# Performance work log

Measured on AMD Instinct MI355X. Metric: run time of the kernel, lower is better.

Reference implementation:

```python
import jax, jax.numpy as jnp
import numpy as np

ENC_H = 512      # encoder_hidden_dim -> encoder_out feature = 2*ENC_H
DEC_H = 512      # decoder_hidden_dim
B, S = 32, 2048  # batch, max_seq_len


def setup_inputs() -> dict:
    key = jax.random.key(0)
    k1, k2, k3, k4, k5, k6, k7 = jax.random.split(key, 7)
    encoder_out = jax.random.normal(k1, (B, S, 2 * ENC_H), dtype=jnp.float32)
    hidden = jax.random.normal(k2, (B, DEC_H), dtype=jnp.float32)
    lengths = jax.random.randint(k3, (B,), 1, S + 1, dtype=jnp.int64)
    in_dim = 2 * ENC_H + DEC_H
    # torch nn.Linear default init scale
    attn_w = jax.random.uniform(k4, (DEC_H, in_dim), jnp.float32, -1.0, 1.0) / np.sqrt(in_dim)
    attn_b = jax.random.uniform(k5, (DEC_H,), jnp.float32, -1.0, 1.0) / np.sqrt(in_dim)
    v_w = jax.random.uniform(k6, (1, DEC_H), jnp.float32, -1.0, 1.0) / np.sqrt(DEC_H)
    v_b = jax.random.uniform(k7, (1,), jnp.float32, -1.0, 1.0) / np.sqrt(DEC_H)
    return {"encoder_out": encoder_out, "hidden": hidden, "lengths": lengths,
            "attn_w": attn_w, "attn_b": attn_b, "v_w": v_w, "v_b": v_b}


def reference(encoder_out, hidden, lengths, attn_w, attn_b, v_w, v_b):
    # encoder_out: [B,S,2E], hidden: [B,D], lengths: [B]
    Bc, Sc, _ = encoder_out.shape
    h = jnp.broadcast_to(hidden[:, None, :], (Bc, Sc, hidden.shape[-1]))
    temp = jnp.concatenate([h, encoder_out], axis=2)           # [B,S,D+2E]
    e = jnp.tanh(jnp.einsum('bsf,df->bsd', temp, attn_w) + attn_b)  # [B,S,D]
    scores = jnp.einsum('bsd,d->bs', e, v_w[0]) + v_b[0]       # [B,S]
    mask = jnp.arange(Sc)[None, :] < lengths[:, None]          # [B,S]
    scores = jnp.where(mask, scores, -jnp.inf)
    energy = jax.nn.softmax(scores, axis=1)                    # softmax over valid positions
    energy = jnp.where(mask, energy, 0.0)                      # padded positions stay exactly 0
    context = jnp.einsum('bs,bse->be', energy, encoder_out)    # [B,2E]
    return context
```

## Files before the change

### kernel.cpp

```cpp
#include <hip/hip_runtime.h>
#include <hip/hip_bf16.h>
#include <math.h>

typedef __attribute__((ext_vector_type(4))) short short4v;
typedef __attribute__((ext_vector_type(8))) short short8;
typedef __attribute__((ext_vector_type(16))) float f32x16;

static constexpr int B  = 32;
static constexpr int S  = 2048;
static constexpr int D  = 512;
static constexpr int KE = 1024;
static constexpr int IN = 1536;

__device__ __forceinline__ unsigned pk2(float lo, float hi) {
    __hip_bfloat162 t = __float22bfloat162_rn(make_float2(lo, hi));
    unsigned u;
    __builtin_memcpy(&u, &t, 4);
    return u;
}

__device__ __forceinline__ short4v pack4(float4 f) {
    unsigned u2[2] = { pk2(f.x, f.y), pk2(f.z, f.w) };
    short4v r;
    __builtin_memcpy(&r, u2, 8);
    return r;
}

__device__ __forceinline__ short8 pack8(float4 f0, float4 f1) {
    unsigned u[4] = { pk2(f0.x, f0.y), pk2(f0.z, f0.w), pk2(f1.x, f1.y), pk2(f1.z, f1.w) };
    short8 r;
    __builtin_memcpy(&r, u, 16);
    return r;
}

__device__ __forceinline__ short8 cat44(short4v lo, short4v hi) {
    short8 r;
    __builtin_memcpy(&r, &lo, 8);
    __builtin_memcpy(((char*)&r) + 8, &hi, 8);
    return r;
}

__device__ __forceinline__ float tanh_fast(float x) {
    float e = __expf(2.0f * x);
    return (e - 1.0f) * __builtin_amdgcn_rcpf(e + 1.0f);
}

__global__ void k_prep(const float* __restrict__ attn_w,
                       const float* __restrict__ hidden,
                       const float* __restrict__ attn_b,
                       unsigned short* __restrict__ Bf,
                       float* __restrict__ u) {
    if (blockIdx.x < 256) {
        int o = blockIdx.x * 256 + threadIdx.x;
        int l6  = o & 63;
        int grp = o >> 6;
        int d = (grp & 15) * 32 + (l6 & 31);
        int k = (grp >> 4) * 16 + (l6 >> 5) * 8;
        const float* src = attn_w + (size_t)d * IN + 512 + k;
        float4 f0 = *(const float4*)src;
        float4 f1 = *(const float4*)(src + 4);
        ((short8*)Bf)[o] = pack8(f0, f1);
    } else {
        int gid = (blockIdx.x - 256) * 256 + threadIdx.x;
        int b = gid >> 9;
        int d = gid & (D - 1);
        const float* h = hidden + b * D;
        const float* w = attn_w + (size_t)d * IN;
        float acc = attn_b[d];
        for (int k = 0; k < D; k += 4) {
            float4 hv = *(const float4*)(h + k);
            float4 wv = *(const float4*)(w + k);
            acc += hv.x * wv.x + hv.y * wv.y + hv.z * wv.z + hv.w * wv.w;
        }
        u[gid] = acc;
    }
}

#define LOADB(K, DST) do {                                     \
    _Pragma("unroll")                                          \
    for (int _jt = 0; _jt < 4; _jt++)                          \
        DST[_jt] = bb[(size_t)(K) * 1024 + _jt * 64];          \
} while (0)

__global__ __launch_bounds__(256, 2) void k_fused(
    const float* __restrict__ enc, const unsigned short* __restrict__ Bfrag,
    const float* __restrict__ u, const float* __restrict__ v_w,
    const float* __restrict__ v_b, const int* __restrict__ lengths,
    float* __restrict__ num, float* __restrict__ den)
{
    __shared__ short4v ldsA[2][64 * 19];
    __shared__ float sPart[4][64];
    __shared__ float sExp[64];

    const int b   = blockIdx.y;
    const int s0  = blockIdx.x * 64;
    const int len = lengths[b];
    if (s0 >= len) return;

    const int tid = threadIdx.x;
    const int w   = tid >> 6;
    const int l   = tid & 63;

    const float* encb = enc + ((size_t)b * S + s0) * KE;
    const int mr = tid >> 4;
    const int cw = tid & 15;
    const float* aG = encb + (size_t)mr * KE + cw * 4;
    const int wbase = mr * 19 + cw;

    const short8* bb = (const short8*)Bfrag + (w * 4) * 64 + l;

    f32x16 acc[2][4];
    #pragma unroll
    for (int mt = 0; mt < 2; mt++)
        #pragma unroll
        for (int jt = 0; jt < 4; jt++)
            #pragma unroll
            for (int e = 0; e < 16; e++) acc[mt][jt][e] = 0.f;

    short8 pb[2][4];
    LOADB(0, pb[0]);
    LOADB(1, pb[1]);

    float4 g[4];
    #pragma unroll
    for (int i = 0; i < 4; i++) g[i] = *(const float4*)(aG + (size_t)i * 16 * KE);

    const int rb0 = (l & 31) * 19 + (l >> 5) * 2;
    const int rb1 = rb0 + 32 * 19;

    #pragma unroll 1
    for (int c = 0; c <= 16; ++c) {
        __syncthreads();
        if (c < 16) {
            #pragma unroll
            for (int i = 0; i < 4; i++)
                ldsA[c & 1][wbase + i * 16 * 19] = pack4(g[i]);
            if (c < 15) {
                #pragma unroll
                for (int i = 0; i < 4; i++)
                    g[i] = *(const float4*)(aG + (size_t)i * 16 * KE + (c + 1) * 64);
            }
        }
        if (c > 0) {
            const int buf = (c - 1) & 1;
            #pragma unroll
            for (int t2 = 0; t2 < 4; ++t2) {
                const short4v* base = &ldsA[buf][t2 * 4];
                short8 a0 = cat44(base[rb0], base[rb0 + 1]);
                short8 a1 = cat44(base[rb1], base[rb1 + 1]);
                const int bp = t2 & 1;
                #pragma unroll
                for (int jt = 0; jt < 4; jt++) {
                    acc[0][jt] = __builtin_amdgcn_mfma_f32_32x32x16_bf16(a0, pb[bp][jt], acc[0][jt], 0, 0, 0);
                    acc[1][jt] = __builtin_amdgcn_mfma_f32_32x32x16_bf16(a1, pb[bp][jt], acc[1][jt], 0, 0, 0);
                }
                LOADB(((c - 1) * 4 + t2 + 2) & 63, pb[bp]);
            }
        }
    }

    float vv[4], uu[4];
    const float* ub = u + b * D;
    #pragma unroll
    for (int jt = 0; jt < 4; jt++) {
        int d = w * 128 + jt * 32 + (l & 31);
        vv[jt] = v_w[d];
        uu[jt] = ub[d];
    }
    float red[2][16];
    #pragma unroll
    for (int mt = 0; mt < 2; mt++)
        #pragma unroll
        for (int r = 0; r < 16; r++) {
            float s = 0.f;
            #pragma unroll
            for (int jt = 0; jt < 4; jt++)
                s += vv[jt] * tanh_fast(acc[mt][jt][r] + uu[jt]);
            red[mt][r] = s;
        }
    #pragma unroll
    for (int off = 16; off >= 1; off >>= 1)
        #pragma unroll
        for (int mt = 0; mt < 2; mt++)
            #pragma unroll
            for (int r = 0; r < 16; r++)
                red[mt][r] += __shfl_xor(red[mt][r], off);
    if ((l & 31) == 0) {
        int hb = (l >> 5) * 4;
        #pragma unroll
        for (int mt = 0; mt < 2; mt++)
            #pragma unroll
            for (int r = 0; r < 16; r++)
                sPart[w][mt * 32 + (r & 3) + 8 * (r >> 2) + hb] = red[mt][r];
    }
    __syncthreads();

    if (tid < 64) {
        float sc = sPart[0][tid] + sPart[1][tid] + sPart[2][tid] + sPart[3][tid] + v_b[0];
        float wexp = (s0 + tid < len) ? __expf(sc) : 0.f;
        sExp[tid] = wexp;
        #pragma unroll
        for (int off = 32; off >= 1; off >>= 1) wexp += __shfl_xor(wexp, off);
        if (tid == 0) atomicAdd(den + b, wexp);
    }
    __syncthreads();

    const float4* e4 = (const float4*)encb;
    float4 cacc[4];
    #pragma unroll
    for (int j = 0; j < 4; j++) cacc[j] = make_float4(0.f, 0.f, 0.f, 0.f);
    #pragma unroll
    for (int i = 0; i < 16; i++) {
        #pragma unroll
        for (int j = 0; j < 4; j++) {
            float wgt = sExp[i * 4 + j];
            float4 v = e4[(size_t)(i * 4 + j) * 256 + tid];
            cacc[j].x += wgt * v.x; cacc[j].y += wgt * v.y;
            cacc[j].z += wgt * v.z; cacc[j].w += wgt * v.w;
        }
    }
    #pragma unroll
    for (int j = 1; j < 4; j++) {
        cacc[0].x += cacc[j].x; cacc[0].y += cacc[j].y;
        cacc[0].z += cacc[j].z; cacc[0].w += cacc[j].w;
    }
    float* o = num + b * KE + tid * 4;
    atomicAdd(o + 0, cacc[0].x);
    atomicAdd(o + 1, cacc[0].y);
    atomicAdd(o + 2, cacc[0].z);
    atomicAdd(o + 3, cacc[0].w);
}

__global__ void k_norm(const float* __restrict__ num, const float* __restrict__ den,
                       float* __restrict__ out) {
    int b = blockIdx.x;
    int t = threadIdx.x;
    float inv = 1.f / den[b];
    float4 v = ((const float4*)(num + b * KE))[t];
    v.x *= inv; v.y *= inv; v.z *= inv; v.w *= inv;
    ((float4*)(out + b * KE))[t] = v;
}

extern "C" void kernel_launch(void* const* d_in, const int* in_sizes, int n_in,
                              void* d_out, int out_size, void* d_ws, size_t ws_size,
                              hipStream_t stream) {
    const float* enc    = (const float*)d_in[0];
    const float* hidden = (const float*)d_in[1];
    const int*   lengths= (const int*)d_in[2];
    const float* attn_w = (const float*)d_in[3];
    const float* attn_b = (const float*)d_in[4];
    const float* v_w    = (const float*)d_in[5];
    const float* v_b    = (const float*)d_in[6];
    float* out = (float*)d_out;

    float* ws  = (float*)d_ws;
    float* u   = ws;
    float* num = u + B * D;
    float* den = num + B * KE;
    unsigned short* Bf = (unsigned short*)(den + 32);

    (void)hipMemsetAsync(num, 0, (size_t)(B * KE + B) * sizeof(float), stream);
    k_prep <<<dim3(320), 256, 0, stream>>>(attn_w, hidden, attn_b, Bf, u);
    k_fused<<<dim3(S / 64, B), 256, 0, stream>>>(enc, Bf, u, v_w, v_b, lengths, num, den);
    k_norm <<<dim3(B), 256, 0, stream>>>(num, den, out);
}
```

Before: 438.8 us.

## Stream encoder tiles into LDS via global_load_lds and coalesce hidden projection

The fused kernel now copies fp32 encoder tiles straight from global memory into a double-buffered, XOR-swizzled LDS buffer using async global_load_lds. The bf16 conversion moves to after the LDS read, which removes the register staging and the pack-then-store step, and the loop prologue/epilogue is simplified. Separately, the hidden·W projection in k_prep is restructured so that 16 lanes cooperatively read contiguous weight rows and combine results with a shuffle reduction, replacing the per-thread strided row loop. The cost is twice the LDS footprint, since tiles are stored as fp32, which could affect occupancy. Correctness also relies on the barrier waiting for the async LDS writes to complete.

```diff
diff --git a/kernel.cpp b/kernel.cpp
--- a/kernel.cpp
+++ b/kernel.cpp
@@ -2,7 +2,6 @@
 #include <hip/hip_bf16.h>
 #include <math.h>
 
-typedef __attribute__((ext_vector_type(4))) short short4v;
 typedef __attribute__((ext_vector_type(8))) short short8;
 typedef __attribute__((ext_vector_type(16))) float f32x16;
 
@@ -19,13 +18,6 @@
     return u;
 }
 
-__device__ __forceinline__ short4v pack4(float4 f) {
-    unsigned u2[2] = { pk2(f.x, f.y), pk2(f.z, f.w) };
-    short4v r;
-    __builtin_memcpy(&r, u2, 8);
-    return r;
-}
-
 __device__ __forceinline__ short8 pack8(float4 f0, float4 f1) {
     unsigned u[4] = { pk2(f0.x, f0.y), pk2(f0.z, f0.w), pk2(f1.x, f1.y), pk2(f1.z, f1.w) };
     short8 r;
@@ -33,16 +25,15 @@
     return r;
 }
 
-__device__ __forceinline__ short8 cat44(short4v lo, short4v hi) {
-    short8 r;
-    __builtin_memcpy(&r, &lo, 8);
-    __builtin_memcpy(((char*)&r) + 8, &hi, 8);
-    return r;
-}
-
 __device__ __forceinline__ float tanh_fast(float x) {
     float e = __expf(2.0f * x);
     return (e - 1.0f) * __builtin_amdgcn_rcpf(e + 1.0f);
+}
+
+typedef const __attribute__((address_space(1))) unsigned int guint;
+typedef __attribute__((address_space(3))) unsigned int luint;
+__device__ __forceinline__ void gload_lds16(const void* g, void* l) {
+    __builtin_amdgcn_global_load_lds((guint*)g, (luint*)l, 16, 0, 0);
 }
 
 __global__ void k_prep(const float* __restrict__ attn_w,
@@ -61,18 +52,31 @@
         float4 f1 = *(const float4*)(src + 4);
         ((short8*)Bf)[o] = pack8(f0, f1);
     } else {
-        int gid = (blockIdx.x - 256) * 256 + threadIdx.x;
-        int b = gid >> 9;
-        int d = gid & (D - 1);
+        int bx = blockIdx.x - 256;
+        int b  = bx >> 1;
+        int dh = bx & 1;
+        int w  = threadIdx.x >> 6;
+        int l  = threadIdx.x & 63;
+        int j  = l & 15;
+        int dsub = l >> 4;
         const float* h = hidden + b * D;
-        const float* w = attn_w + (size_t)d * IN;
-        float acc = attn_b[d];
-        for (int k = 0; k < D; k += 4) {
-            float4 hv = *(const float4*)(h + k);
-            float4 wv = *(const float4*)(w + k);
-            acc += hv.x * wv.x + hv.y * wv.y + hv.z * wv.z + hv.w * wv.w;
-        }
-        u[gid] = acc;
+        float4 hv[8];
+        #pragma unroll
+        for (int i = 0; i < 8; i++) hv[i] = *(const float4*)(h + i * 64 + j * 4);
+        #pragma unroll
+        for (int p = 0; p < 16; p++) {
+            int d = dh * 256 + p * 16 + w * 4 + dsub;
+            const float* wr = attn_w + (size_t)d * IN + j * 4;
+            float a = 0.f;
+            #pragma unroll
+            for (int i = 0; i < 8; i++) {
+                float4 wv = *(const float4*)(wr + i * 64);
+                a += hv[i].x * wv.x + hv[i].y * wv.y + hv[i].z * wv.z + hv[i].w * wv.w;
+            }
+            #pragma unroll
+            for (int off = 8; off >= 1; off >>= 1) a += __shfl_xor(a, off);
+            if (j == 0) u[b * D + d] = a + attn_b[d];
+        }
     }
 }
 
@@ -88,7 +92,7 @@
     const float* __restrict__ v_b, const int* __restrict__ lengths,
     float* __restrict__ num, float* __restrict__ den)
 {
-    __shared__ short4v ldsA[2][64 * 19];
+    __shared__ float4 ldsA[2][1024];
     __shared__ float sPart[4][64];
     __shared__ float sExp[64];
 
@@ -102,10 +106,10 @@
     const int l   = tid & 63;
 
     const float* encb = enc + ((size_t)b * S + s0) * KE;
-    const int mr = tid >> 4;
-    const int cw = tid & 15;
-    const float* aG = encb + (size_t)mr * KE + cw * 4;
-    const int wbase = mr * 19 + cw;
+
+    const int rsub = l >> 4;
+    const int xorv = (l & 15) ^ (w * 4 + rsub);
+    const float* aSrc = encb + (size_t)(w * 4 + rsub) * KE + 4 * xorv;
 
     const short8* bb = (const short8*)Bfrag + (w * 4) * 64 + l;
 
@@ -121,41 +125,43 @@
     LOADB(0, pb[0]);
     LOADB(1, pb[1]);
 
-    float4 g[4];
-    #pragma unroll
-    for (int i = 0; i < 4; i++) g[i] = *(const float4*)(aG + (size_t)i * 16 * KE);
-
-    const int rb0 = (l & 31) * 19 + (l >> 5) * 2;
-    const int rb1 = rb0 + 32 * 19;
+    const int m0  = l & 31;
+    const int x15 = m0 & 15;
+    const int hi2 = (l >> 5) * 2;
+
+    #pragma unroll
+    for (int i = 0; i < 4; i++)
+        gload_lds16(aSrc + (size_t)i * 16 * KE, (void*)&ldsA[0][(i * 4 + w) * 64]);
 
     #pragma unroll 1
-    for (int c = 0; c <= 16; ++c) {
+    for (int c = 0; c < 16; ++c) {
         __syncthreads();
-        if (c < 16) {
+        if (c < 15) {
+            const float* src = aSrc + (c + 1) * 64;
+            float4* bufn = ldsA[(c + 1) & 1];
             #pragma unroll
             for (int i = 0; i < 4; i++)
-                ldsA[c & 1][wbase + i * 16 * 19] = pack4(g[i]);
-            if (c < 15) {
-                #pragma unroll
-                for (int i = 0; i < 4; i++)
-                    g[i] = *(const float4*)(aG + (size_t)i * 16 * KE + (c + 1) * 64);
+                gload_lds16(src + (size_t)i * 16 * KE, (void*)&bufn[(i * 4 + w) * 64]);
+        }
+        const float4* bf = (const float4*)ldsA[c & 1];
+        #pragma unroll
+        for (int t2 = 0; t2 < 4; ++t2) {
+            const int sq = t2 * 4 + hi2;
+            const int p0 = sq ^ x15;
+            const int p1 = (sq + 1) ^ x15;
+            float4 f00 = bf[m0 * 16 + p0];
+            float4 f01 = bf[m0 * 16 + p1];
+            float4 f10 = bf[(m0 + 32) * 16 + p0];
+            float4 f11 = bf[(m0 + 32) * 16 + p1];
+            short8 a0 = pack8(f00, f01);
+            short8 a1 = pack8(f10, f11);
+            const int bp = t2 & 1;
+            #pragma unroll
+            for (int jt = 0; jt < 4; jt++) {
+                acc[0][jt] = __builtin_amdgcn_mfma_f32_32x32x16_bf16(a0, pb[bp][jt], acc[0][jt], 0, 0, 0);
+                acc[1][jt] = __builtin_amdgcn_mfma_f32_32x32x16_bf16(a1, pb[bp][jt], acc[1][jt], 0, 0, 0);
             }
-        }
-        if (c > 0) {
-            const int buf = (c - 1) & 1;
-            #pragma unroll
-            for (int t2 = 0; t2 < 4; ++t2) {
-                const short4v* base = &ldsA[buf][t2 * 4];
-                short8 a0 = cat44(base[rb0], base[rb0 + 1]);
-                short8 a1 = cat44(base[rb1], base[rb1 + 1]);
-                const int bp = t2 & 1;
-                #pragma unroll
-                for (int jt = 0; jt < 4; jt++) {
-                    acc[0][jt] = __builtin_amdgcn_mfma_f32_32x32x16_bf16(a0, pb[bp][jt], acc[0][jt], 0, 0, 0);
-                    acc[1][jt] = __builtin_amdgcn_mfma_f32_32x32x16_bf16(a1, pb[bp][jt], acc[1][jt], 0, 0, 0);
-                }
-                LOADB(((c - 1) * 4 + t2 + 2) & 63, pb[bp]);
-            }
+            LOADB((c * 4 + t2 + 2) & 63, pb[bp]);
         }
     }
 
```

Result: no change. 444.9 us (+1.4%).
